# Optimization experiments

Measured on AMD Instinct MI355X. Metric: run time of the kernel, lower is better.

Reference implementation:

```python
import jax, jax.numpy as jnp
import numpy as np

LAMBDA_OTDL = 1.0


def _emd2_1d(p, q):
    """Exact EMD^2 (squared-distance cost on integer grid) between two 1D
    histograms p, q of length D. For convex cost |i-j|^2 on a line the optimal
    plan is the monotone (quantile) coupling, so
      EMD2 = int_0^1 (F_p^{-1}(t) - F_q^{-1}(t))^2 dt,
    matching ot.emd2 with M[i,j] = |i-j|^2 exactly."""
    D = p.shape[0]
    cp = jnp.cumsum(p)
    cq = jnp.cumsum(q)
    t = jnp.sort(jnp.concatenate([cp, cq]))          # [2D] merged CDF breakpoints
    dt = jnp.diff(t, prepend=jnp.zeros((1,), t.dtype))
    tm = t - 0.5 * dt                                 # segment midpoints
    ip = jnp.clip(jnp.searchsorted(cp, tm, side='left'), 0, D - 1)
    iq = jnp.clip(jnp.searchsorted(cq, tm, side='left'), 0, D - 1)
    return jnp.sum(dt * (ip - iq).astype(p.dtype) ** 2)


def setup_inputs() -> dict:
    key = jax.random.key(0)
    k1, k2 = jax.random.split(key)
    B, C, D, W = 65536, 1, 256, 1
    P = jax.random.uniform(k1, (B, C, D, W), dtype=jnp.float32)
    Q = jax.random.uniform(k2, (B, C, D, W), dtype=jnp.float32)
    return {"P": P, "Q": Q}


def reference(P, Q):
    B = P.shape[0]
    P_prime = P / jnp.sum(P, axis=(2, 3), keepdims=True)
    Q_prime = Q / jnp.sum(Q, axis=(2, 3), keepdims=True)
    p_flat = P_prime.reshape(B, -1)   # [B, D] since C=W=1
    q_flat = Q_prime.reshape(B, -1)
    OT_values = jax.vmap(_emd2_1d)(p_flat, q_flat)          # [B]
    OT_values = jax.lax.stop_gradient(OT_values)            # original detaches (numpy solver)
    mse_loss = jnp.mean((P - Q) ** 2, axis=(1, 2, 3))       # [B]
    loss = mse_loss + LAMBDA_OTDL * OT_values
    return jnp.mean(loss)
```

## Files before the change

### kernel.cpp

```cpp
#include <hip/hip_runtime.h>
#include <hip/hip_fp16.h>


#define NW    4
#define DSZ   256
#define LROW  264

template <int CTRL, int RMASK, bool BC>
__device__ __forceinline__ float dpp_add(float x) {
    int t = __builtin_amdgcn_update_dpp(0, __float_as_int(x), CTRL, RMASK, 0xf, BC);
    return x + __int_as_float(t);
}

__device__ __forceinline__ float half_scan(float x) {
    x = dpp_add<0x111, 0xf, true >(x);
    x = dpp_add<0x112, 0xf, true >(x);
    x = dpp_add<0x114, 0xf, true >(x);
    x = dpp_add<0x118, 0xf, true >(x);
    x = dpp_add<0x142, 0xa, false>(x);
    return x;
}

__device__ __forceinline__ float rdlane31(float x) {
    return __int_as_float(__builtin_amdgcn_readlane(__float_as_int(x), 31));
}
__device__ __forceinline__ float rdlane63(float x) {
    return __int_as_float(__builtin_amdgcn_readlane(__float_as_int(x), 63));
}

__device__ __forceinline__ unsigned int f2h(float x) {
    return (unsigned int)__half_as_ushort(__float2half(x));
}
__device__ __forceinline__ float h2f(unsigned int x) {
    return __half2float(__ushort_as_half((unsigned short)x));
}

__device__ __forceinline__ float fe_stage(
    const float4 pA, const float4 pB, const float4 qA, const float4 qB,
    unsigned short* cp, unsigned short* cq, int l32, bool hiHalf)
{
    float d0 = pA.x - qA.x, d1 = pA.y - qA.y, d2 = pA.z - qA.z, d3 = pA.w - qA.w;
    float d4 = pB.x - qB.x, d5 = pB.y - qB.y, d6 = pB.z - qB.z, d7 = pB.w - qB.w;
    float msel = d0*d0 + d1*d1 + d2*d2 + d3*d3 + d4*d4 + d5*d5 + d6*d6 + d7*d7;

    float pl = (pA.x + pA.y + pA.z + pA.w) + (pB.x + pB.y + pB.z + pB.w);
    float ql = (qA.x + qA.y + qA.z + qA.w) + (qB.x + qB.y + qB.z + qB.w);
    float ps = half_scan(pl);
    float qs = half_scan(ql);

    float ptot = hiHalf ? rdlane63(ps) : rdlane31(ps);
    float qtot = hiHalf ? rdlane63(qs) : rdlane31(qs);
    float rp = __builtin_amdgcn_rcpf(ptot);
    float rq = __builtin_amdgcn_rcpf(qtot);
    float pe = ps - pl, qe = qs - ql;

    float p0 = pe + pA.x, p1 = p0 + pA.y, p2 = p1 + pA.z, p3 = p2 + pA.w;
    float p4 = p3 + pB.x, p5 = p4 + pB.y, p6 = p5 + pB.z;
    float q0 = qe + qA.x, q1 = q0 + qA.y, q2 = q1 + qA.z, q3 = q2 + qA.w;
    float q4 = q3 + qB.x, q5 = q4 + qB.y, q6 = q5 + qB.z;

    uint4 wp, wq;
    wp.x = f2h(p0 * rp) | (f2h(p1 * rp) << 16);
    wp.y = f2h(p2 * rp) | (f2h(p3 * rp) << 16);
    wp.z = f2h(p4 * rp) | (f2h(p5 * rp) << 16);
    wp.w = f2h(p6 * rp) | (f2h(ps * rp) << 16);
    wq.x = f2h(q0 * rq) | (f2h(q1 * rq) << 16);
    wq.y = f2h(q2 * rq) | (f2h(q3 * rq) << 16);
    wq.z = f2h(q4 * rq) | (f2h(q5 * rq) << 16);
    wq.w = f2h(q6 * rq) | (f2h(qs * rq) << 16);

    *reinterpret_cast<uint4*>(&cp[l32 * 8]) = wp;
    *reinterpret_cast<uint4*>(&cq[l32 * 8]) = wq;
    return msel;
}

__global__ __launch_bounds__(256, 6) void otdl_main(
    const float* __restrict__ P, const float* __restrict__ Q,
    double* __restrict__ partial, int B, int bpw)
{
    __shared__ unsigned short s_cp[NW][2][2][LROW];
    __shared__ unsigned short s_cq[NW][2][2][LROW];
    __shared__ double s_bsum[NW];

    const int tid  = threadIdx.x;
    const int wv   = tid >> 6;
    const int lane = tid & 63;
    const int l32  = lane & 31;
    const bool hiHalf = (lane >= 32);
    const int rh   = hiHalf ? 1 : 0;
    const int wgl  = blockIdx.x * NW + wv;

    if (lane == 0) {
#pragma unroll
        for (int bf = 0; bf < 2; ++bf)
#pragma unroll
            for (int r2 = 0; r2 < 2; ++r2) {
                s_cp[wv][bf][r2][DSZ] = 0x4000;
                s_cq[wv][bf][r2][DSZ] = 0x4000;
            }
    }

    double acc = 0.0;
    const int  k0      = l32 * 16;
    const int  npair   = (bpw + 1) >> 1;
    const long rowbase = (long)wgl * bpw;
    const bool isLast  = (l32 == 31);

    float4 pA, pB, qA, qB;
    {
        long b = rowbase + rh;
        long c = (b < B) ? b : (B - 1);
        const float4* Pr = reinterpret_cast<const float4*>(P + c * DSZ + l32 * 8);
        const float4* Qr = reinterpret_cast<const float4*>(Q + c * DSZ + l32 * 8);
        pA = Pr[0]; pB = Pr[1];
        qA = Qr[0]; qB = Qr[1];
    }

    float mselC = fe_stage(pA, pB, qA, qB, s_cp[wv][0][rh], s_cq[wv][0][rh],
                           l32, hiHalf);
    if (npair > 1) {
        long b = rowbase + 2 + rh;
        long c = (b < B) ? b : (B - 1);
        const float4* Pr = reinterpret_cast<const float4*>(P + c * DSZ + l32 * 8);
        const float4* Qr = reinterpret_cast<const float4*>(Q + c * DSZ + l32 * 8);
        pA = Pr[0]; pB = Pr[1];
        qA = Qr[0]; qB = Qr[1];
    }

#pragma unroll 2
    for (int p = 0; p < npair; ++p) {
        const int cur = p & 1;

        float mselN = 0.0f;
        if (p + 1 < npair) {
            mselN = fe_stage(pA, pB, qA, qB,
                             s_cp[wv][cur ^ 1][rh], s_cq[wv][cur ^ 1][rh],
                             l32, hiHalf);
        }
        if (p + 2 < npair) {
            long b = rowbase + 2 * (p + 2) + rh;
            long c = (b < B) ? b : (B - 1);
            const float4* Pr = reinterpret_cast<const float4*>(P + c * DSZ + l32 * 8);
            const float4* Qr = reinterpret_cast<const float4*>(Q + c * DSZ + l32 * 8);
            pA = Pr[0]; pB = Pr[1];
            qA = Qr[0]; qB = Qr[1];
        }

        const unsigned short* cp = s_cp[wv][cur][rh];
        const unsigned short* cq = s_cq[wv][cur][rh];

        int lo = k0 > DSZ ? k0 - DSZ : 0;
        int hi = k0 < DSZ ? k0 : DSZ;
#pragma unroll
        for (int s = 0; s < 9; ++s) {
            int mid = (lo + hi) >> 1;
            int jm  = k0 - 1 - mid;
            int jr  = jm < 0 ? 0 : jm;
            unsigned int qq = cq[jr];
            unsigned int cc = cp[mid];
            bool pred = (jm < 0) || (qq <= cc);
            hi = pred ? mid : hi;
            lo = pred ? lo  : mid + 1;
        }

        const unsigned short* pA_ = cp + lo;
        const unsigned short* pB_ = cq + (k0 - lo);
        float u  = (float)(4 * lo - 2 * k0 - 1);
        unsigned int a  = pA_[0];
        unsigned int b2 = pB_[0];
        unsigned int an = pA_[1];
        unsigned int bn = pB_[1];
        float e_ = 0.0f;
#pragma unroll
        for (int s = 0; s < 16; ++s) {
            bool  ea   = a < b2;
            float val  = h2f(ea ? a : b2);
            float u2   = u + 2.0f;
            float coef = ea ? -u2 : u;
            e_ = fmaf(val, coef, e_);
            u  = ea ? u2 : (u - 2.0f);
            pA_ += ea ? 1 : 0;
            pB_ += ea ? 0 : 1;
            a  = ea ? an : a;
            b2 = ea ? b2 : bn;
            an = pA_[1];
            bn = pB_[1];
        }

        e_ -= isLast ? fabsf(h2f(cp[DSZ - 1]) - h2f(cq[DSZ - 1])) : 0.0f;

        if (rowbase + 2 * p + rh < B)
            acc += (double)(e_ + mselC * (1.0f / 256.0f));
        mselC = mselN;
    }

#pragma unroll
    for (int off = 32; off; off >>= 1) {
        double o = __shfl_xor(acc, off, 64);
        acc += o;
    }
    if (lane == 0) s_bsum[wv] = acc;
    __syncthreads();
    if (tid == 0) {
        partial[blockIdx.x] = s_bsum[0] + s_bsum[1] + s_bsum[2] + s_bsum[3];
    }
}

__global__ __launch_bounds__(256) void otdl_reduce(
    const double* __restrict__ partial, int n, float* __restrict__ out, double invB)
{
    __shared__ double sdata[256];
    double a = 0.0;
    for (int i = threadIdx.x; i < n; i += 256) a += partial[i];
    sdata[threadIdx.x] = a;
    __syncthreads();
    for (int s2 = 128; s2 > 0; s2 >>= 1) {
        if (threadIdx.x < s2) sdata[threadIdx.x] += sdata[threadIdx.x + s2];
        __syncthreads();
    }
    if (threadIdx.x == 0) out[0] = (float)(sdata[0] * invB);
}

extern "C" void kernel_launch(void* const* d_in, const int* in_sizes, int n_in,
                              void* d_out, int out_size, void* d_ws, size_t ws_size,
                              hipStream_t stream)
{
    const float* P = (const float*)d_in[0];
    const float* Q = (const float*)d_in[1];
    float* out = (float*)d_out;
    double* partial = (double*)d_ws;

    int B = in_sizes[0] / DSZ;
    const int blocks = 2048;
    const int totalWaves = blocks * NW;
    int bpw = (B + totalWaves - 1) / totalWaves;

    otdl_main<<<blocks, 256, 0, stream>>>(P, Q, partial, B, bpw);
    otdl_reduce<<<1, 256, 0, stream>>>(partial, blocks, out, 1.0 / (double)B);
}
```

Before: 38.97 us.

## Interleave next-pair co-rank binary search with current-pair merge loop

Software-pipelines the per-lane co-rank binary search: the search for the next row pair runs interleaved with the 16-step merge of the current pair, and its result is carried to the next iteration. This lets the serial, dependent LDS loads of the binary search overlap with the independent merge chain to hide LDS latency. It adds a prologue search, more live registers, and on the last iteration a wasted search on an unwritten buffer.

Result: slower. 69.92 us (+79.4%).

```diff
diff --git a/kernel.cpp b/kernel.cpp
--- a/kernel.cpp
+++ b/kernel.cpp
@@ -74,105 +74,35 @@
     return msel;
 }
 
-__global__ __launch_bounds__(256, 6) void otdl_main(
-    const float* __restrict__ P, const float* __restrict__ Q,
-    double* __restrict__ partial, int B, int bpw)
-{
-    __shared__ unsigned short s_cp[NW][2][2][LROW];
-    __shared__ unsigned short s_cq[NW][2][2][LROW];
-    __shared__ double s_bsum[NW];
-
-    const int tid  = threadIdx.x;
-    const int wv   = tid >> 6;
-    const int lane = tid & 63;
-    const int l32  = lane & 31;
-    const bool hiHalf = (lane >= 32);
-    const int rh   = hiHalf ? 1 : 0;
-    const int wgl  = blockIdx.x * NW + wv;
-
-    if (lane == 0) {
-#pragma unroll
-        for (int bf = 0; bf < 2; ++bf)
-#pragma unroll
-            for (int r2 = 0; r2 < 2; ++r2) {
-                s_cp[wv][bf][r2][DSZ] = 0x4000;
-                s_cq[wv][bf][r2][DSZ] = 0x4000;
-            }
-    }
-
-    double acc = 0.0;
-    const int  k0      = l32 * 16;
-    const int  npair   = (bpw + 1) >> 1;
-    const long rowbase = (long)wgl * bpw;
-    const bool isLast  = (l32 == 31);
-
-    float4 pA, pB, qA, qB;
-    {
-        long b = rowbase + rh;
-        long c = (b < B) ? b : (B - 1);
-        const float4* Pr = reinterpret_cast<const float4*>(P + c * DSZ + l32 * 8);
-        const float4* Qr = reinterpret_cast<const float4*>(Q + c * DSZ + l32 * 8);
-        pA = Pr[0]; pB = Pr[1];
-        qA = Qr[0]; qB = Qr[1];
-    }
-
-    float mselC = fe_stage(pA, pB, qA, qB, s_cp[wv][0][rh], s_cq[wv][0][rh],
-                           l32, hiHalf);
-    if (npair > 1) {
-        long b = rowbase + 2 + rh;
-        long c = (b < B) ? b : (B - 1);
-        const float4* Pr = reinterpret_cast<const float4*>(P + c * DSZ + l32 * 8);
-        const float4* Qr = reinterpret_cast<const float4*>(Q + c * DSZ + l32 * 8);
-        pA = Pr[0]; pB = Pr[1];
-        qA = Qr[0]; qB = Qr[1];
-    }
-
-#pragma unroll 2
-    for (int p = 0; p < npair; ++p) {
-        const int cur = p & 1;
-
-        float mselN = 0.0f;
-        if (p + 1 < npair) {
-            mselN = fe_stage(pA, pB, qA, qB,
-                             s_cp[wv][cur ^ 1][rh], s_cq[wv][cur ^ 1][rh],
-                             l32, hiHalf);
-        }
-        if (p + 2 < npair) {
-            long b = rowbase + 2 * (p + 2) + rh;
-            long c = (b < B) ? b : (B - 1);
-            const float4* Pr = reinterpret_cast<const float4*>(P + c * DSZ + l32 * 8);
-            const float4* Qr = reinterpret_cast<const float4*>(Q + c * DSZ + l32 * 8);
-            pA = Pr[0]; pB = Pr[1];
-            qA = Qr[0]; qB = Qr[1];
-        }
-
-        const unsigned short* cp = s_cp[wv][cur][rh];
-        const unsigned short* cq = s_cq[wv][cur][rh];
-
-        int lo = k0 > DSZ ? k0 - DSZ : 0;
-        int hi = k0 < DSZ ? k0 : DSZ;
-#pragma unroll
-        for (int s = 0; s < 9; ++s) {
+__device__ __forceinline__ float corank_merge(
+    const unsigned short* cpN, const unsigned short* cqN,
+    const unsigned short* cpC, const unsigned short* cqC,
+    int k0, int loC, bool isLast, int& loN)
+{
+    int lo = k0 > DSZ ? k0 - DSZ : 0;
+    int hi = k0 < DSZ ? k0 : DSZ;
+
+    const unsigned short* pA_ = cpC + loC;
+    const unsigned short* pB_ = cqC + (k0 - loC);
+    float u  = (float)(4 * loC - 2 * k0 - 1);
+    unsigned int a  = pA_[0];
+    unsigned int b2 = pB_[0];
+    unsigned int an = pA_[1];
+    unsigned int bn = pB_[1];
+    float e_ = 0.0f;
+#pragma unroll
+    for (int s = 0; s < 16; ++s) {
+        if (s < 9) {
             int mid = (lo + hi) >> 1;
             int jm  = k0 - 1 - mid;
             int jr  = jm < 0 ? 0 : jm;
-            unsigned int qq = cq[jr];
-            unsigned int cc = cp[mid];
+            unsigned int qq = cqN[jr];
+            unsigned int cc = cpN[mid];
             bool pred = (jm < 0) || (qq <= cc);
             hi = pred ? mid : hi;
             lo = pred ? lo  : mid + 1;
         }
-
-        const unsigned short* pA_ = cp + lo;
-        const unsigned short* pB_ = cq + (k0 - lo);
-        float u  = (float)(4 * lo - 2 * k0 - 1);
-        unsigned int a  = pA_[0];
-        unsigned int b2 = pB_[0];
-        unsigned int an = pA_[1];
-        unsigned int bn = pB_[1];
-        float e_ = 0.0f;
-#pragma unroll
-        for (int s = 0; s < 16; ++s) {
+        {
             bool  ea   = a < b2;
             float val  = h2f(ea ? a : b2);
             float u2   = u + 2.0f;
@@ -186,12 +116,112 @@
             an = pA_[1];
             bn = pB_[1];
         }
-
-        e_ -= isLast ? fabsf(h2f(cp[DSZ - 1]) - h2f(cq[DSZ - 1])) : 0.0f;
+    }
+    loN = lo;
+    e_ -= isLast ? fabsf(h2f(cpC[DSZ - 1]) - h2f(cqC[DSZ - 1])) : 0.0f;
+    return e_;
+}
+
+__global__ __launch_bounds__(256, 6) void otdl_main(
+    const float* __restrict__ P, const float* __restrict__ Q,
+    double* __restrict__ partial, int B, int bpw)
+{
+    __shared__ unsigned short s_cp[NW][2][2][LROW];
+    __shared__ unsigned short s_cq[NW][2][2][LROW];
+    __shared__ double s_bsum[NW];
+
+    const int tid  = threadIdx.x;
+    const int wv   = tid >> 6;
+    const int lane = tid & 63;
+    const int l32  = lane & 31;
+    const bool hiHalf = (lane >= 32);
+    const int rh   = hiHalf ? 1 : 0;
+    const int wgl  = blockIdx.x * NW + wv;
+
+    if (lane == 0) {
+#pragma unroll
+        for (int bf = 0; bf < 2; ++bf)
+#pragma unroll
+            for (int r2 = 0; r2 < 2; ++r2) {
+                s_cp[wv][bf][r2][DSZ] = 0x4000;
+                s_cq[wv][bf][r2][DSZ] = 0x4000;
+            }
+    }
+
+    double acc = 0.0;
+    const int  k0      = l32 * 16;
+    const int  npair   = (bpw + 1) >> 1;
+    const long rowbase = (long)wgl * bpw;
+    const bool isLast  = (l32 == 31);
+
+    float4 pA, pB, qA, qB;
+    {
+        long b = rowbase + rh;
+        long c = (b < B) ? b : (B - 1);
+        const float4* Pr = reinterpret_cast<const float4*>(P + c * DSZ + l32 * 8);
+        const float4* Qr = reinterpret_cast<const float4*>(Q + c * DSZ + l32 * 8);
+        pA = Pr[0]; pB = Pr[1];
+        qA = Qr[0]; qB = Qr[1];
+    }
+
+    float mselC = fe_stage(pA, pB, qA, qB, s_cp[wv][0][rh], s_cq[wv][0][rh],
+                           l32, hiHalf);
+    if (npair > 1) {
+        long b = rowbase + 2 + rh;
+        long c = (b < B) ? b : (B - 1);
+        const float4* Pr = reinterpret_cast<const float4*>(P + c * DSZ + l32 * 8);
+        const float4* Qr = reinterpret_cast<const float4*>(Q + c * DSZ + l32 * 8);
+        pA = Pr[0]; pB = Pr[1];
+        qA = Qr[0]; qB = Qr[1];
+    }
+    int loC;
+    {
+        const unsigned short* cp = s_cp[wv][0][rh];
+        const unsigned short* cq = s_cq[wv][0][rh];
+        int lo = k0 > DSZ ? k0 - DSZ : 0;
+        int hi = k0 < DSZ ? k0 : DSZ;
+#pragma unroll
+        for (int s = 0; s < 9; ++s) {
+            int mid = (lo + hi) >> 1;
+            int jm  = k0 - 1 - mid;
+            int jr  = jm < 0 ? 0 : jm;
+            unsigned int qq = cq[jr];
+            unsigned int cc = cp[mid];
+            bool pred = (jm < 0) || (qq <= cc);
+            hi = pred ? mid : hi;
+            lo = pred ? lo  : mid + 1;
+        }
+        loC = lo;
+    }
+
+#pragma unroll 2
+    for (int p = 0; p < npair; ++p) {
+        const int cur = p & 1;
+        unsigned short* cpN = s_cp[wv][cur ^ 1][rh];
+        unsigned short* cqN = s_cq[wv][cur ^ 1][rh];
+        const unsigned short* cpC = s_cp[wv][cur][rh];
+        const unsigned short* cqC = s_cq[wv][cur][rh];
+
+        float mselN = 0.0f;
+        if (p + 1 < npair) {
+            mselN = fe_stage(pA, pB, qA, qB, cpN, cqN, l32, hiHalf);
+        }
+        if (p + 2 < npair) {
+            long b = rowbase + 2 * (p + 2) + rh;
+            long c = (b < B) ? b : (B - 1);
+            const float4* Pr = reinterpret_cast<const float4*>(P + c * DSZ + l32 * 8);
+            const float4* Qr = reinterpret_cast<const float4*>(Q + c * DSZ + l32 * 8);
+            pA = Pr[0]; pB = Pr[1];
+            qA = Qr[0]; qB = Qr[1];
+        }
+
+        int loN;
+        float e_ = corank_merge(cpN, cqN, cpC, cqC, k0, loC, isLast, loN);
 
         if (rowbase + 2 * p + rh < B)
             acc += (double)(e_ + mselC * (1.0f / 256.0f));
         mselC = mselN;
+        loC   = loN;
     }
 
 #pragma unroll
```

## Replace merge-path binary search with bitonic merge of packed CDF keys

Applied to the files above, without the earlier changes.

Replaces the per-lane merge-path binary search and serial 16-step merge of the two CDF arrays with a register bitonic merge. Each lane packs fp16 CDF values with index tags into 32-bit keys, and the merge runs over a half-wave using ds_swizzle and DPP exchanges plus in-register compare-exchange stages. The EMD contribution is then read directly from the sorted positions. The change also drops LDS double buffering and the one-row-ahead fe_stage software pipeline, and removes the launch_bounds occupancy hint. This trades data-dependent LDS reads for many more ALU and cross-lane operations, and may cost overlap and occupancy.

Result: slower. 45.11 us (+15.8%).

```diff
diff --git a/kernel.cpp b/kernel.cpp
--- a/kernel.cpp
+++ b/kernel.cpp
@@ -33,6 +33,12 @@
 }
 __device__ __forceinline__ float h2f(unsigned int x) {
     return __half2float(__ushort_as_half((unsigned short)x));
+}
+
+__device__ __forceinline__ unsigned ce_sel(unsigned v, unsigned o, bool lower) {
+    unsigned mn = v < o ? v : o;
+    unsigned mx = v < o ? o : v;
+    return lower ? mn : mx;
 }
 
 __device__ __forceinline__ float fe_stage(
@@ -74,12 +80,12 @@
     return msel;
 }
 
-__global__ __launch_bounds__(256, 6) void otdl_main(
+__global__ void otdl_main(
     const float* __restrict__ P, const float* __restrict__ Q,
     double* __restrict__ partial, int B, int bpw)
 {
-    __shared__ unsigned short s_cp[NW][2][2][LROW];
-    __shared__ unsigned short s_cq[NW][2][2][LROW];
+    __shared__ __align__(16) unsigned short s_cp[NW][2][LROW];
+    __shared__ __align__(16) unsigned short s_cq[NW][2][LROW];
     __shared__ double s_bsum[NW];
 
     const int tid  = threadIdx.x;
@@ -90,21 +96,9 @@
     const int rh   = hiHalf ? 1 : 0;
     const int wgl  = blockIdx.x * NW + wv;
 
-    if (lane == 0) {
-#pragma unroll
-        for (int bf = 0; bf < 2; ++bf)
-#pragma unroll
-            for (int r2 = 0; r2 < 2; ++r2) {
-                s_cp[wv][bf][r2][DSZ] = 0x4000;
-                s_cq[wv][bf][r2][DSZ] = 0x4000;
-            }
-    }
-
     double acc = 0.0;
-    const int  k0      = l32 * 16;
     const int  npair   = (bpw + 1) >> 1;
     const long rowbase = (long)wgl * bpw;
-    const bool isLast  = (l32 == 31);
 
     float4 pA, pB, qA, qB;
     {
@@ -116,29 +110,15 @@
         qA = Qr[0]; qB = Qr[1];
     }
 
-    float mselC = fe_stage(pA, pB, qA, qB, s_cp[wv][0][rh], s_cq[wv][0][rh],
-                           l32, hiHalf);
-    if (npair > 1) {
-        long b = rowbase + 2 + rh;
-        long c = (b < B) ? b : (B - 1);
-        const float4* Pr = reinterpret_cast<const float4*>(P + c * DSZ + l32 * 8);
-        const float4* Qr = reinterpret_cast<const float4*>(Q + c * DSZ + l32 * 8);
-        pA = Pr[0]; pB = Pr[1];
-        qA = Qr[0]; qB = Qr[1];
-    }
-
-#pragma unroll 2
     for (int p = 0; p < npair; ++p) {
-        const int cur = p & 1;
-
-        float mselN = 0.0f;
+        unsigned short* cp = s_cp[wv][rh];
+        unsigned short* cq = s_cq[wv][rh];
+
+        float msel = fe_stage(pA, pB, qA, qB, cp, cq, l32, hiHalf);
+        long bcur = rowbase + 2 * p + rh;
+
         if (p + 1 < npair) {
-            mselN = fe_stage(pA, pB, qA, qB,
-                             s_cp[wv][cur ^ 1][rh], s_cq[wv][cur ^ 1][rh],
-                             l32, hiHalf);
-        }
-        if (p + 2 < npair) {
-            long b = rowbase + 2 * (p + 2) + rh;
+            long b = rowbase + 2 * (p + 1) + rh;
             long c = (b < B) ? b : (B - 1);
             const float4* Pr = reinterpret_cast<const float4*>(P + c * DSZ + l32 * 8);
             const float4* Qr = reinterpret_cast<const float4*>(Q + c * DSZ + l32 * 8);
@@ -146,52 +126,117 @@
             qA = Qr[0]; qB = Qr[1];
         }
 
-        const unsigned short* cp = s_cp[wv][cur][rh];
-        const unsigned short* cq = s_cq[wv][cur][rh];
-
-        int lo = k0 > DSZ ? k0 - DSZ : 0;
-        int hi = k0 < DSZ ? k0 : DSZ;
-#pragma unroll
-        for (int s = 0; s < 9; ++s) {
-            int mid = (lo + hi) >> 1;
-            int jm  = k0 - 1 - mid;
-            int jr  = jm < 0 ? 0 : jm;
-            unsigned int qq = cq[jr];
-            unsigned int cc = cp[mid];
-            bool pred = (jm < 0) || (qq <= cc);
-            hi = pred ? mid : hi;
-            lo = pred ? lo  : mid + 1;
-        }
-
-        const unsigned short* pA_ = cp + lo;
-        const unsigned short* pB_ = cq + (k0 - lo);
-        float u  = (float)(4 * lo - 2 * k0 - 1);
-        unsigned int a  = pA_[0];
-        unsigned int b2 = pB_[0];
-        unsigned int an = pA_[1];
-        unsigned int bn = pB_[1];
+        unsigned v[16];
+        if (l32 < 16) {
+            const uint4* w = reinterpret_cast<const uint4*>(cp);
+            uint4 a = w[2 * l32], b = w[2 * l32 + 1];
+            unsigned i0 = 16 * l32 + 0x100u;
+            v[0] = ((a.x & 0xFFFFu) << 16) | (i0 + 0);
+            v[1] = (a.x & 0xFFFF0000u)     | (i0 + 1);
+            v[2] = ((a.y & 0xFFFFu) << 16) | (i0 + 2);
+            v[3] = (a.y & 0xFFFF0000u)     | (i0 + 3);
+            v[4] = ((a.z & 0xFFFFu) << 16) | (i0 + 4);
+            v[5] = (a.z & 0xFFFF0000u)     | (i0 + 5);
+            v[6] = ((a.w & 0xFFFFu) << 16) | (i0 + 6);
+            v[7] = (a.w & 0xFFFF0000u)     | (i0 + 7);
+            v[8] = ((b.x & 0xFFFFu) << 16) | (i0 + 8);
+            v[9] = (b.x & 0xFFFF0000u)     | (i0 + 9);
+            v[10] = ((b.y & 0xFFFFu) << 16) | (i0 + 10);
+            v[11] = (b.y & 0xFFFF0000u)     | (i0 + 11);
+            v[12] = ((b.z & 0xFFFFu) << 16) | (i0 + 12);
+            v[13] = (b.z & 0xFFFF0000u)     | (i0 + 13);
+            v[14] = ((b.w & 0xFFFFu) << 16) | (i0 + 14);
+            v[15] = (b.w & 0xFFFF0000u)     | (i0 + 15);
+        } else {
+            const uint4* w = reinterpret_cast<const uint4*>(cq);
+            uint4 a = w[62 - 2 * l32], b = w[63 - 2 * l32];
+            unsigned j0 = 496 - 16 * l32;
+            v[0]  = (b.w & 0xFFFF0000u)     | (j0 + 15);
+            v[1]  = ((b.w & 0xFFFFu) << 16) | (j0 + 14);
+            v[2]  = (b.z & 0xFFFF0000u)     | (j0 + 13);
+            v[3]  = ((b.z & 0xFFFFu) << 16) | (j0 + 12);
+            v[4]  = (b.y & 0xFFFF0000u)     | (j0 + 11);
+            v[5]  = ((b.y & 0xFFFFu) << 16) | (j0 + 10);
+            v[6]  = (b.x & 0xFFFF0000u)     | (j0 + 9);
+            v[7]  = ((b.x & 0xFFFFu) << 16) | (j0 + 8);
+            v[8]  = (a.w & 0xFFFF0000u)     | (j0 + 7);
+            v[9]  = ((a.w & 0xFFFFu) << 16) | (j0 + 6);
+            v[10] = (a.z & 0xFFFF0000u)     | (j0 + 5);
+            v[11] = ((a.z & 0xFFFFu) << 16) | (j0 + 4);
+            v[12] = (a.y & 0xFFFF0000u)     | (j0 + 3);
+            v[13] = ((a.y & 0xFFFFu) << 16) | (j0 + 2);
+            v[14] = (a.x & 0xFFFF0000u)     | (j0 + 1);
+            v[15] = ((a.x & 0xFFFFu) << 16) | (j0 + 0);
+        }
+
+        const bool lw16 = (l32 & 16) == 0;
+        const bool lw8  = (l32 & 8)  == 0;
+        const bool lw4  = (l32 & 4)  == 0;
+        const bool lw2  = (l32 & 2)  == 0;
+        const bool lw1  = (l32 & 1)  == 0;
+#pragma unroll
+        for (int e = 0; e < 16; ++e) {
+            unsigned o = (unsigned)__builtin_amdgcn_ds_swizzle((int)v[e], 0x401F);
+            v[e] = ce_sel(v[e], o, lw16);
+        }
+#pragma unroll
+        for (int e = 0; e < 16; ++e) {
+            unsigned o = (unsigned)__builtin_amdgcn_ds_swizzle((int)v[e], 0x201F);
+            v[e] = ce_sel(v[e], o, lw8);
+        }
+#pragma unroll
+        for (int e = 0; e < 16; ++e) {
+            unsigned o = (unsigned)__builtin_amdgcn_ds_swizzle((int)v[e], 0x101F);
+            v[e] = ce_sel(v[e], o, lw4);
+        }
+#pragma unroll
+        for (int e = 0; e < 16; ++e) {
+            unsigned o = (unsigned)__builtin_amdgcn_update_dpp(0, (int)v[e], 0x4E, 0xF, 0xF, false);
+            v[e] = ce_sel(v[e], o, lw2);
+        }
+#pragma unroll
+        for (int e = 0; e < 16; ++e) {
+            unsigned o = (unsigned)__builtin_amdgcn_update_dpp(0, (int)v[e], 0xB1, 0xF, 0xF, false);
+            v[e] = ce_sel(v[e], o, lw1);
+        }
+#pragma unroll
+        for (int e = 0; e < 8; ++e) {
+            unsigned x = v[e], y = v[e + 8];
+            v[e] = x < y ? x : y;  v[e + 8] = x < y ? y : x;
+        }
+#pragma unroll
+        for (int g = 0; g < 16; g += 8)
+#pragma unroll
+            for (int e = g; e < g + 4; ++e) {
+                unsigned x = v[e], y = v[e + 4];
+                v[e] = x < y ? x : y;  v[e + 4] = x < y ? y : x;
+            }
+#pragma unroll
+        for (int g = 0; g < 16; g += 4)
+#pragma unroll
+            for (int e = g; e < g + 2; ++e) {
+                unsigned x = v[e], y = v[e + 2];
+                v[e] = x < y ? x : y;  v[e + 2] = x < y ? y : x;
+            }
+#pragma unroll
+        for (int e = 0; e < 16; e += 2) {
+            unsigned x = v[e], y = v[e + 1];
+            v[e] = x < y ? x : y;  v[e + 1] = x < y ? y : x;
+        }
+
         float e_ = 0.0f;
-#pragma unroll
-        for (int s = 0; s < 16; ++s) {
-            bool  ea   = a < b2;
-            float val  = h2f(ea ? a : b2);
-            float u2   = u + 2.0f;
-            float coef = ea ? -u2 : u;
-            e_ = fmaf(val, coef, e_);
-            u  = ea ? u2 : (u - 2.0f);
-            pA_ += ea ? 1 : 0;
-            pB_ += ea ? 0 : 1;
-            a  = ea ? an : a;
-            b2 = ea ? b2 : bn;
-            an = pA_[1];
-            bn = pB_[1];
-        }
-
-        e_ -= isLast ? fabsf(h2f(cp[DSZ - 1]) - h2f(cq[DSZ - 1])) : 0.0f;
-
-        if (rowbase + 2 * p + rh < B)
-            acc += (double)(e_ + mselC * (1.0f / 256.0f));
-        mselC = mselN;
+        const int k2 = l32 * 32;
+#pragma unroll
+        for (int e = 0; e < 16; ++e) {
+            unsigned pl = v[e];
+            int idx = (int)(pl & 0xFFu);
+            float val = h2f(pl >> 16);
+            int ci = (k2 + 2 * e) - 4 * idx - 1;
+            float cf = (idx == 255) ? 0.0f : (float)ci;
+            e_ = fmaf(val, cf, e_);
+        }
+
+        if (bcur < B) acc += (double)(e_ + msel * (1.0f / 256.0f));
     }
 
 #pragma unroll
```
